# Kernel tuning notes

Measured on AMD Instinct MI355X. Metric: run time of the kernel, lower is better.

Reference implementation:

```python
import jax, jax.numpy as jnp
import numpy as np


def setup_inputs() -> dict:
    key = jax.random.key(0)
    k1, k2 = jax.random.split(key)
    B, Te, Td, D = 16, 1024, 1024, 1024
    encoder_outputs = jax.random.normal(k1, (B, Te, D), dtype=jnp.float32)
    decoder_outputs = jax.random.normal(k2, (B, Td, D), dtype=jnp.float32)
    return {"encoder_outputs": encoder_outputs, "decoder_outputs": decoder_outputs}


def reference(encoder_outputs, decoder_outputs):
    # Luong score: [B, Te, Td] = enc @ dec^T
    luong_score = jnp.einsum("bed,btd->bet", encoder_outputs, decoder_outputs)
    # softmax over encoder-time axis (axis=1), matching K.softmax(..., axis=1)
    attn = jax.nn.softmax(luong_score, axis=1)
    # context vector: sum over encoder time of enc * attn -> [B, Td, D]
    # (original materializes [B, Te, Td, D]; this einsum is the same math)
    encoder_vector = jnp.einsum("bed,bet->btd", encoder_outputs, attn)
    return jnp.concatenate([decoder_outputs, encoder_vector], axis=-1)
```

## Files before the change

kernel.cpp:

```cpp
#include <hip/hip_runtime.h>
#include <hip/hip_bf16.h>
#include <stdint.h>

typedef __bf16 bf16x8 __attribute__((ext_vector_type(8)));
typedef float f32x4 __attribute__((ext_vector_type(4)));

#define B_DIM 16
#define TD 1024
#define TE 1024
#define DD 1024

__device__ __forceinline__ uint32_t rne_bf16(float x) {
  uint32_t u = __builtin_bit_cast(uint32_t, x);
  return (u + 0x7FFFu + ((u >> 16) & 1u)) >> 16;
}

__global__ __launch_bounds__(256, 2)
void k1_scores(const float* __restrict__ dec, const float* __restrict__ enc,
               float* __restrict__ out) {
  __shared__ uint32_t AhU[2048], AlU[2048], BhU[2048], BlU[2048];
  const int tid = threadIdx.x;
  const int lane = tid & 63;
  const int wave = tid >> 6;
  const int wm = wave >> 1, wn = wave & 1;
  const int b = blockIdx.z;
  const int t0 = blockIdx.y * 128, e0 = blockIdx.x * 128;
  const float* A = dec + (size_t)b * TD * DD;
  const float* Bm = enc + (size_t)b * TE * DD;

  const int r = tid >> 3, c4 = tid & 7;
  const float* aptr = A + (size_t)(t0 + r) * DD + c4 * 4;
  const float* bptr = Bm + (size_t)(e0 + r) * DD + c4 * 4;

  const int lr = lane & 15, q = lane >> 4;
  int aoff[4], boff[4];
#pragma unroll
  for (int i = 0; i < 4; ++i) {
    aoff[i] = (wm * 64 + i * 16 + lr) * 16 + q * 4;
    boff[i] = (wn * 64 + i * 16 + lr) * 16 + q * 4;
  }

  f32x4 acc[4][4] = {};

  for (int k0 = 0; k0 < DD; k0 += 32) {
#pragma unroll
    for (int s = 0; s < 4; ++s) {
      const float4 va = *(const float4*)(aptr + (size_t)(32 * s) * DD);
      const float4 vb = *(const float4*)(bptr + (size_t)(32 * s) * DD);
      const int woff = (r + 32 * s) * 16 + c4 * 2;
      {
        uint32_t u0 = __builtin_bit_cast(uint32_t, va.x);
        uint32_t u1 = __builtin_bit_cast(uint32_t, va.y);
        uint32_t u2 = __builtin_bit_cast(uint32_t, va.z);
        uint32_t u3 = __builtin_bit_cast(uint32_t, va.w);
        uint32_t m0 = u0 & 0xFFFF0000u, m1 = u1 & 0xFFFF0000u;
        uint32_t m2 = u2 & 0xFFFF0000u, m3 = u3 & 0xFFFF0000u;
        float l0 = va.x - __builtin_bit_cast(float, m0);
        float l1 = va.y - __builtin_bit_cast(float, m1);
        float l2 = va.z - __builtin_bit_cast(float, m2);
        float l3 = va.w - __builtin_bit_cast(float, m3);
        *(uint2*)&AhU[woff] = make_uint2((m0 >> 16) | m1, (m2 >> 16) | m3);
        *(uint2*)&AlU[woff] = make_uint2(
            (__builtin_bit_cast(uint32_t, l0) >> 16) |
                (__builtin_bit_cast(uint32_t, l1) & 0xFFFF0000u),
            (__builtin_bit_cast(uint32_t, l2) >> 16) |
                (__builtin_bit_cast(uint32_t, l3) & 0xFFFF0000u));
      }
      {
        uint32_t u0 = __builtin_bit_cast(uint32_t, vb.x);
        uint32_t u1 = __builtin_bit_cast(uint32_t, vb.y);
        uint32_t u2 = __builtin_bit_cast(uint32_t, vb.z);
        uint32_t u3 = __builtin_bit_cast(uint32_t, vb.w);
        uint32_t m0 = u0 & 0xFFFF0000u, m1 = u1 & 0xFFFF0000u;
        uint32_t m2 = u2 & 0xFFFF0000u, m3 = u3 & 0xFFFF0000u;
        float l0 = vb.x - __builtin_bit_cast(float, m0);
        float l1 = vb.y - __builtin_bit_cast(float, m1);
        float l2 = vb.z - __builtin_bit_cast(float, m2);
        float l3 = vb.w - __builtin_bit_cast(float, m3);
        *(uint2*)&BhU[woff] = make_uint2((m0 >> 16) | m1, (m2 >> 16) | m3);
        *(uint2*)&BlU[woff] = make_uint2(
            (__builtin_bit_cast(uint32_t, l0) >> 16) |
                (__builtin_bit_cast(uint32_t, l1) & 0xFFFF0000u),
            (__builtin_bit_cast(uint32_t, l2) >> 16) |
                (__builtin_bit_cast(uint32_t, l3) & 0xFFFF0000u));
      }
    }
    __syncthreads();

    bf16x8 ah[4], al[4];
#pragma unroll
    for (int mi = 0; mi < 4; ++mi) {
      ah[mi] = *(const bf16x8*)&AhU[aoff[mi]];
      al[mi] = *(const bf16x8*)&AlU[aoff[mi]];
    }
#pragma unroll
    for (int ni = 0; ni < 4; ++ni) {
      bf16x8 bh = *(const bf16x8*)&BhU[boff[ni]];
      bf16x8 bl = *(const bf16x8*)&BlU[boff[ni]];
#pragma unroll
      for (int mi = 0; mi < 4; ++mi) {
        f32x4 c = acc[mi][ni];
        c = __builtin_amdgcn_mfma_f32_16x16x32_bf16(al[mi], bh, c, 0, 0, 0);
        c = __builtin_amdgcn_mfma_f32_16x16x32_bf16(ah[mi], bl, c, 0, 0, 0);
        c = __builtin_amdgcn_mfma_f32_16x16x32_bf16(ah[mi], bh, c, 0, 0, 0);
        acc[mi][ni] = c;
      }
    }
    __syncthreads();
    aptr += 32;
    bptr += 32;
  }

  float* outb = out + (size_t)b * TD * 2048 + 1024;
  const int tb = t0 + wm * 64 + q * 4;
  const int eb = e0 + wn * 64 + lr;
#pragma unroll
  for (int mi = 0; mi < 4; ++mi)
#pragma unroll
    for (int ni = 0; ni < 4; ++ni)
#pragma unroll
      for (int i = 0; i < 4; ++i)
        outb[(size_t)(tb + mi * 16 + i) * 2048 + (eb + ni * 16)] = acc[mi][ni][i];
}

__global__ __launch_bounds__(256)
void k2_softmax(float* out) {
  const int lane = threadIdx.x & 63;
  const int row = blockIdx.x * 4 + (threadIdx.x >> 6);
  float* Srow = out + (size_t)row * 2048 + 1024;
  float4 v[4];
#pragma unroll
  for (int s = 0; s < 4; ++s) v[s] = *(const float4*)(Srow + lane * 4 + s * 256);
  float m = -1e30f;
#pragma unroll
  for (int s = 0; s < 4; ++s)
    m = fmaxf(m, fmaxf(fmaxf(v[s].x, v[s].y), fmaxf(v[s].z, v[s].w)));
#pragma unroll
  for (int o = 32; o > 0; o >>= 1) m = fmaxf(m, __shfl_xor(m, o));
  float e[16];
  float sum = 0.f;
#pragma unroll
  for (int s = 0; s < 4; ++s) {
    e[4 * s + 0] = __expf(v[s].x - m);
    e[4 * s + 1] = __expf(v[s].y - m);
    e[4 * s + 2] = __expf(v[s].z - m);
    e[4 * s + 3] = __expf(v[s].w - m);
    sum += e[4 * s + 0] + e[4 * s + 1] + e[4 * s + 2] + e[4 * s + 3];
  }
#pragma unroll
  for (int o = 32; o > 0; o >>= 1) sum += __shfl_xor(sum, o);
  const float inv = 1.0f / sum;
  uint32_t* Prow = (uint32_t*)(out + (size_t)row * 2048);
#pragma unroll
  for (int s = 0; s < 4; ++s) {
    uint32_t r0 = rne_bf16(e[4 * s + 0] * inv);
    uint32_t r1 = rne_bf16(e[4 * s + 1] * inv);
    uint32_t r2 = rne_bf16(e[4 * s + 2] * inv);
    uint32_t r3 = rne_bf16(e[4 * s + 3] * inv);
    *(uint2*)&Prow[lane * 2 + s * 128] =
        make_uint2(r0 | (r1 << 16), r2 | (r3 << 16));
  }
}

__global__ __launch_bounds__(256, 2)
void k3_av(const float* __restrict__ enc, float* __restrict__ out) {
  __shared__ uint32_t AU[2048];
  __shared__ uint32_t BtU[128 * 20];
  const int tid = threadIdx.x;
  const int lane = tid & 63, wave = tid >> 6;
  const int wm = wave >> 1, wn = wave & 1;
  const int b = blockIdx.z;
  const int t0 = blockIdx.y * 128, d0 = blockIdx.x * 128;
  const float* V = enc + (size_t)b * TE * DD;
  const uint16_t* Pb = (const uint16_t*)(out + (size_t)b * TD * 2048);
  const int lr = lane & 15, q = lane >> 4;
  int aoff[4], boff[4];
#pragma unroll
  for (int i = 0; i < 4; ++i) {
    aoff[i] = (wm * 64 + i * 16 + lr) * 16 + q * 4;
    boff[i] = (wn * 64 + i * 16 + lr) * 20 + q * 4;
  }
  const int dB = tid & 127;
  f32x4 acc[4][4] = {};

  for (int e0k = 0; e0k < TE; e0k += 32) {
#pragma unroll
    for (int s = 0; s < 2; ++s) {
      int c = tid + 256 * s;
      int rc = c >> 2, cc = c & 3;
      uint4 va = *(const uint4*)(Pb + (size_t)(t0 + rc) * 4096 + e0k + cc * 8);
      *(uint4*)&AU[c * 4] = va;
    }
#pragma unroll
    for (int s = 0; s < 4; ++s) {
      int eg = (tid >> 7) + 2 * s;
      const float* src = V + (size_t)(e0k + eg * 4) * DD + d0 + dB;
      float x0 = src[0], x1 = src[DD], x2 = src[2 * DD], x3 = src[3 * DD];
      uint32_t r0 = rne_bf16(x0), r1 = rne_bf16(x1);
      uint32_t r2 = rne_bf16(x2), r3 = rne_bf16(x3);
      *(uint2*)&BtU[dB * 20 + eg * 2] =
          make_uint2(r0 | (r1 << 16), r2 | (r3 << 16));
    }
    __syncthreads();

    bf16x8 af[4];
#pragma unroll
    for (int mi = 0; mi < 4; ++mi) af[mi] = *(const bf16x8*)&AU[aoff[mi]];
#pragma unroll
    for (int ni = 0; ni < 4; ++ni) {
      bf16x8 bfr = *(const bf16x8*)&BtU[boff[ni]];
#pragma unroll
      for (int mi = 0; mi < 4; ++mi)
        acc[mi][ni] =
            __builtin_amdgcn_mfma_f32_16x16x32_bf16(af[mi], bfr, acc[mi][ni], 0, 0, 0);
    }
    __syncthreads();
  }

  float* outb = out + (size_t)b * TD * 2048 + 1024;
  const int tb = t0 + wm * 64 + q * 4;
  const int db = d0 + wn * 64 + lr;
#pragma unroll
  for (int mi = 0; mi < 4; ++mi)
#pragma unroll
    for (int ni = 0; ni < 4; ++ni)
#pragma unroll
      for (int i = 0; i < 4; ++i)
        outb[(size_t)(tb + mi * 16 + i) * 2048 + (db + ni * 16)] = acc[mi][ni][i];
}

__global__ __launch_bounds__(256)
void k4_copydec(const float4* __restrict__ dec4, float4* __restrict__ out4) {
  size_t g = (size_t)blockIdx.x * 512 + threadIdx.x;
#pragma unroll
  for (int s = 0; s < 2; ++s, g += 256) {
    size_t row = g >> 8, col = g & 255;
    out4[row * 512 + col] = dec4[g];
  }
}

extern "C" void kernel_launch(void* const* d_in, const int* in_sizes, int n_in,
                              void* d_out, int out_size, void* d_ws, size_t ws_size,
                              hipStream_t stream) {
  const float* enc = (const float*)d_in[0];
  const float* dec = (const float*)d_in[1];
  float* out = (float*)d_out;

  hipLaunchKernelGGL(k1_scores, dim3(8, 8, 16), dim3(256), 0, stream, dec, enc, out);
  hipLaunchKernelGGL(k2_softmax, dim3(4096), dim3(256), 0, stream, out);
  hipLaunchKernelGGL(k3_av, dim3(8, 8, 16), dim3(256), 0, stream, enc, out);
  hipLaunchKernelGGL(k4_copydec, dim3(8192), dim3(256), 0, stream,
                     (const float4*)dec, (float4*)out);
}
```

Baseline: 443.3 us.

## Switch score GEMM from split-bf16 to single fp16 MFMA, restructure AV loads

The scores GEMM no longer splits inputs into hi/lo bf16 parts and runs three MFMAs per tile. It converts to fp16 with round-toward-zero packing and runs a single f16 MFMA, cutting matrix work and LDS traffic to about a third. Softmax probabilities and the V operand in the AV kernel also move to fp16. The AV kernel reads P fragments straight from global memory instead of staging them in LDS, and loads V with float4 loads into a padded transposed LDS tile. The trade is lower score precision: fp16 with RTZ loses accuracy relative to the three-term bf16 split, and score magnitudes around 32 then feed exp, which risks exceeding the tolerance.

```diff
diff --git a/kernel.cpp b/kernel.cpp
--- a/kernel.cpp
+++ b/kernel.cpp
@@ -2,7 +2,8 @@
 #include <hip/hip_bf16.h>
 #include <stdint.h>
 
-typedef __bf16 bf16x8 __attribute__((ext_vector_type(8)));
+typedef _Float16 f16x8 __attribute__((ext_vector_type(8)));
+typedef __fp16 fp16x2 __attribute__((ext_vector_type(2)));
 typedef float f32x4 __attribute__((ext_vector_type(4)));
 
 #define B_DIM 16
@@ -10,101 +11,57 @@
 #define TE 1024
 #define DD 1024
 
-__device__ __forceinline__ uint32_t rne_bf16(float x) {
-  uint32_t u = __builtin_bit_cast(uint32_t, x);
-  return (u + 0x7FFFu + ((u >> 16) & 1u)) >> 16;
+__device__ __forceinline__ uint32_t pk2(float a, float b) {
+  fp16x2 h = __builtin_amdgcn_cvt_pkrtz(a, b);
+  return __builtin_bit_cast(uint32_t, h);
 }
 
 __global__ __launch_bounds__(256, 2)
 void k1_scores(const float* __restrict__ dec, const float* __restrict__ enc,
                float* __restrict__ out) {
-  __shared__ uint32_t AhU[2048], AlU[2048], BhU[2048], BlU[2048];
-  const int tid = threadIdx.x;
-  const int lane = tid & 63;
-  const int wave = tid >> 6;
+  __shared__ uint32_t AS[128 * 20], BS[128 * 20];
+  const int tid = threadIdx.x, lane = tid & 63, wave = tid >> 6;
   const int wm = wave >> 1, wn = wave & 1;
   const int b = blockIdx.z;
   const int t0 = blockIdx.y * 128, e0 = blockIdx.x * 128;
   const float* A = dec + (size_t)b * TD * DD;
   const float* Bm = enc + (size_t)b * TE * DD;
 
-  const int r = tid >> 3, c4 = tid & 7;
-  const float* aptr = A + (size_t)(t0 + r) * DD + c4 * 4;
-  const float* bptr = Bm + (size_t)(e0 + r) * DD + c4 * 4;
+  const int r0 = tid >> 3, c4 = tid & 7;
+  const float* aptr = A + (size_t)(t0 + r0) * DD + c4 * 4;
+  const float* bptr = Bm + (size_t)(e0 + r0) * DD + c4 * 4;
+  const int wls = r0 * 20 + c4 * 2;
 
   const int lr = lane & 15, q = lane >> 4;
   int aoff[4], boff[4];
 #pragma unroll
   for (int i = 0; i < 4; ++i) {
-    aoff[i] = (wm * 64 + i * 16 + lr) * 16 + q * 4;
-    boff[i] = (wn * 64 + i * 16 + lr) * 16 + q * 4;
+    aoff[i] = (wm * 64 + i * 16 + lr) * 20 + q * 4;
+    boff[i] = (wn * 64 + i * 16 + lr) * 20 + q * 4;
   }
 
   f32x4 acc[4][4] = {};
 
   for (int k0 = 0; k0 < DD; k0 += 32) {
 #pragma unroll
-    for (int s = 0; s < 4; ++s) {
-      const float4 va = *(const float4*)(aptr + (size_t)(32 * s) * DD);
-      const float4 vb = *(const float4*)(bptr + (size_t)(32 * s) * DD);
-      const int woff = (r + 32 * s) * 16 + c4 * 2;
-      {
-        uint32_t u0 = __builtin_bit_cast(uint32_t, va.x);
-        uint32_t u1 = __builtin_bit_cast(uint32_t, va.y);
-        uint32_t u2 = __builtin_bit_cast(uint32_t, va.z);
-        uint32_t u3 = __builtin_bit_cast(uint32_t, va.w);
-        uint32_t m0 = u0 & 0xFFFF0000u, m1 = u1 & 0xFFFF0000u;
-        uint32_t m2 = u2 & 0xFFFF0000u, m3 = u3 & 0xFFFF0000u;
-        float l0 = va.x - __builtin_bit_cast(float, m0);
-        float l1 = va.y - __builtin_bit_cast(float, m1);
-        float l2 = va.z - __builtin_bit_cast(float, m2);
-        float l3 = va.w - __builtin_bit_cast(float, m3);
-        *(uint2*)&AhU[woff] = make_uint2((m0 >> 16) | m1, (m2 >> 16) | m3);
-        *(uint2*)&AlU[woff] = make_uint2(
-            (__builtin_bit_cast(uint32_t, l0) >> 16) |
-                (__builtin_bit_cast(uint32_t, l1) & 0xFFFF0000u),
-            (__builtin_bit_cast(uint32_t, l2) >> 16) |
-                (__builtin_bit_cast(uint32_t, l3) & 0xFFFF0000u));
-      }
-      {
-        uint32_t u0 = __builtin_bit_cast(uint32_t, vb.x);
-        uint32_t u1 = __builtin_bit_cast(uint32_t, vb.y);
-        uint32_t u2 = __builtin_bit_cast(uint32_t, vb.z);
-        uint32_t u3 = __builtin_bit_cast(uint32_t, vb.w);
-        uint32_t m0 = u0 & 0xFFFF0000u, m1 = u1 & 0xFFFF0000u;
-        uint32_t m2 = u2 & 0xFFFF0000u, m3 = u3 & 0xFFFF0000u;
-        float l0 = vb.x - __builtin_bit_cast(float, m0);
-        float l1 = vb.y - __builtin_bit_cast(float, m1);
-        float l2 = vb.z - __builtin_bit_cast(float, m2);
-        float l3 = vb.w - __builtin_bit_cast(float, m3);
-        *(uint2*)&BhU[woff] = make_uint2((m0 >> 16) | m1, (m2 >> 16) | m3);
-        *(uint2*)&BlU[woff] = make_uint2(
-            (__builtin_bit_cast(uint32_t, l0) >> 16) |
-                (__builtin_bit_cast(uint32_t, l1) & 0xFFFF0000u),
-            (__builtin_bit_cast(uint32_t, l2) >> 16) |
-                (__builtin_bit_cast(uint32_t, l3) & 0xFFFF0000u));
-      }
+    for (int j = 0; j < 4; ++j) {
+      const float4 va = *(const float4*)(aptr + (size_t)(32 * j) * DD);
+      const float4 vb = *(const float4*)(bptr + (size_t)(32 * j) * DD);
+      *(uint2*)&AS[wls + j * 640] = make_uint2(pk2(va.x, va.y), pk2(va.z, va.w));
+      *(uint2*)&BS[wls + j * 640] = make_uint2(pk2(vb.x, vb.y), pk2(vb.z, vb.w));
     }
     __syncthreads();
 
-    bf16x8 ah[4], al[4];
-#pragma unroll
-    for (int mi = 0; mi < 4; ++mi) {
-      ah[mi] = *(const bf16x8*)&AhU[aoff[mi]];
-      al[mi] = *(const bf16x8*)&AlU[aoff[mi]];
-    }
+    f16x8 af[4];
+#pragma unroll
+    for (int mi = 0; mi < 4; ++mi) af[mi] = *(const f16x8*)&AS[aoff[mi]];
 #pragma unroll
     for (int ni = 0; ni < 4; ++ni) {
-      bf16x8 bh = *(const bf16x8*)&BhU[boff[ni]];
-      bf16x8 bl = *(const bf16x8*)&BlU[boff[ni]];
-#pragma unroll
-      for (int mi = 0; mi < 4; ++mi) {
-        f32x4 c = acc[mi][ni];
-        c = __builtin_amdgcn_mfma_f32_16x16x32_bf16(al[mi], bh, c, 0, 0, 0);
-        c = __builtin_amdgcn_mfma_f32_16x16x32_bf16(ah[mi], bl, c, 0, 0, 0);
-        c = __builtin_amdgcn_mfma_f32_16x16x32_bf16(ah[mi], bh, c, 0, 0, 0);
-        acc[mi][ni] = c;
-      }
+      f16x8 bf = *(const f16x8*)&BS[boff[ni]];
+#pragma unroll
+      for (int mi = 0; mi < 4; ++mi)
+        acc[mi][ni] =
+            __builtin_amdgcn_mfma_f32_16x16x32_f16(af[mi], bf, acc[mi][ni], 0, 0, 0);
     }
     __syncthreads();
     aptr += 32;
@@ -153,68 +110,65 @@
   uint32_t* Prow = (uint32_t*)(out + (size_t)row * 2048);
 #pragma unroll
   for (int s = 0; s < 4; ++s) {
-    uint32_t r0 = rne_bf16(e[4 * s + 0] * inv);
-    uint32_t r1 = rne_bf16(e[4 * s + 1] * inv);
-    uint32_t r2 = rne_bf16(e[4 * s + 2] * inv);
-    uint32_t r3 = rne_bf16(e[4 * s + 3] * inv);
     *(uint2*)&Prow[lane * 2 + s * 128] =
-        make_uint2(r0 | (r1 << 16), r2 | (r3 << 16));
+        make_uint2(pk2(e[4 * s + 0] * inv, e[4 * s + 1] * inv),
+                   pk2(e[4 * s + 2] * inv, e[4 * s + 3] * inv));
   }
 }
 
 __global__ __launch_bounds__(256, 2)
 void k3_av(const float* __restrict__ enc, float* __restrict__ out) {
-  __shared__ uint32_t AU[2048];
-  __shared__ uint32_t BtU[128 * 20];
-  const int tid = threadIdx.x;
-  const int lane = tid & 63, wave = tid >> 6;
+  __shared__ uint32_t BS[128 * 18];
+  const int tid = threadIdx.x, lane = tid & 63, wave = tid >> 6;
   const int wm = wave >> 1, wn = wave & 1;
   const int b = blockIdx.z;
   const int t0 = blockIdx.y * 128, d0 = blockIdx.x * 128;
   const float* V = enc + (size_t)b * TE * DD;
-  const uint16_t* Pb = (const uint16_t*)(out + (size_t)b * TD * 2048);
+  const _Float16* Pb = (const _Float16*)(out + (size_t)b * TD * 2048);
+
   const int lr = lane & 15, q = lane >> 4;
-  int aoff[4], boff[4];
-#pragma unroll
-  for (int i = 0; i < 4; ++i) {
-    aoff[i] = (wm * 64 + i * 16 + lr) * 16 + q * 4;
-    boff[i] = (wn * 64 + i * 16 + lr) * 20 + q * 4;
-  }
-  const int dB = tid & 127;
+  size_t arow[4];
+#pragma unroll
+  for (int i = 0; i < 4; ++i)
+    arow[i] = (size_t)(t0 + wm * 64 + i * 16 + lr) * 4096 + q * 8;
+  int boffd[4];
+#pragma unroll
+  for (int i = 0; i < 4; ++i) boffd[i] = (wn * 64 + i * 16 + lr) * 18 + q * 4;
+
+  const int eq = tid & 7, u = (tid >> 3) & 31;
+  const float* vptr = V + (size_t)(eq * 4) * DD + d0 + u * 4;
+  const int wbase = (u * 4) * 18 + eq * 2;
+
   f32x4 acc[4][4] = {};
 
   for (int e0k = 0; e0k < TE; e0k += 32) {
-#pragma unroll
-    for (int s = 0; s < 2; ++s) {
-      int c = tid + 256 * s;
-      int rc = c >> 2, cc = c & 3;
-      uint4 va = *(const uint4*)(Pb + (size_t)(t0 + rc) * 4096 + e0k + cc * 8);
-      *(uint4*)&AU[c * 4] = va;
-    }
-#pragma unroll
-    for (int s = 0; s < 4; ++s) {
-      int eg = (tid >> 7) + 2 * s;
-      const float* src = V + (size_t)(e0k + eg * 4) * DD + d0 + dB;
-      float x0 = src[0], x1 = src[DD], x2 = src[2 * DD], x3 = src[3 * DD];
-      uint32_t r0 = rne_bf16(x0), r1 = rne_bf16(x1);
-      uint32_t r2 = rne_bf16(x2), r3 = rne_bf16(x3);
-      *(uint2*)&BtU[dB * 20 + eg * 2] =
-          make_uint2(r0 | (r1 << 16), r2 | (r3 << 16));
-    }
-    __syncthreads();
-
-    bf16x8 af[4];
-#pragma unroll
-    for (int mi = 0; mi < 4; ++mi) af[mi] = *(const bf16x8*)&AU[aoff[mi]];
+    const float4 v0 = *(const float4*)(vptr + 0 * (size_t)DD);
+    const float4 v1 = *(const float4*)(vptr + 1 * (size_t)DD);
+    const float4 v2 = *(const float4*)(vptr + 2 * (size_t)DD);
+    const float4 v3 = *(const float4*)(vptr + 3 * (size_t)DD);
+    *(uint2*)&BS[wbase + 0 * 18] = make_uint2(pk2(v0.x, v1.x), pk2(v2.x, v3.x));
+    *(uint2*)&BS[wbase + 1 * 18] = make_uint2(pk2(v0.y, v1.y), pk2(v2.y, v3.y));
+    *(uint2*)&BS[wbase + 2 * 18] = make_uint2(pk2(v0.z, v1.z), pk2(v2.z, v3.z));
+    *(uint2*)&BS[wbase + 3 * 18] = make_uint2(pk2(v0.w, v1.w), pk2(v2.w, v3.w));
+    __syncthreads();
+
+    f16x8 af[4];
+#pragma unroll
+    for (int mi = 0; mi < 4; ++mi)
+      af[mi] = *(const f16x8*)(Pb + arow[mi] + e0k);
 #pragma unroll
     for (int ni = 0; ni < 4; ++ni) {
-      bf16x8 bfr = *(const bf16x8*)&BtU[boff[ni]];
+      const uint2 lo = *(const uint2*)&BS[boffd[ni]];
+      const uint2 hi = *(const uint2*)&BS[boffd[ni] + 2];
+      const uint4 bb = make_uint4(lo.x, lo.y, hi.x, hi.y);
+      const f16x8 bf = __builtin_bit_cast(f16x8, bb);
 #pragma unroll
       for (int mi = 0; mi < 4; ++mi)
         acc[mi][ni] =
-            __builtin_amdgcn_mfma_f32_16x16x32_bf16(af[mi], bfr, acc[mi][ni], 0, 0, 0);
+            __builtin_amdgcn_mfma_f32_16x16x32_f16(af[mi], bf, acc[mi][ni], 0, 0, 0);
     }
     __syncthreads();
+    vptr += 32 * (size_t)DD;
   }
 
   float* outb = out + (size_t)b * TD * 2048 + 1024;
```

Measured after the change: 492.0 us. 1.11x slower.
